# Performance work log

Measured on AMD Instinct MI355X. Metric: run time of the kernel, lower is better.

## Reference

```python
import jax, jax.numpy as jnp
import numpy as np

N, K, C, CL = 1024, 32, 64, 128
H = 2 * C  # MLP hidden = 2 * pair channels


def _ln(x, g, b, eps=1e-5):
    m = x.mean(-1, keepdims=True)
    v = jnp.mean(jnp.square(x - m), -1, keepdims=True)
    return (x - m) * jax.lax.rsqrt(v + eps) * g + b


def setup_inputs() -> dict:
    key = jax.random.key(0)
    ks = jax.random.split(key, 16)

    def w(k, shape):
        return jax.random.normal(k, shape, jnp.float32) / np.float32(np.sqrt(shape[0]))

    local = jax.random.normal(ks[0], (N, CL), jnp.float32)
    pair = jax.random.normal(ks[1], (N, N, C), jnp.float32)
    pair_update = jax.random.normal(ks[2], (N, K, C), jnp.float32)
    r = jax.random.randint(ks[3], (N, K), -(N // 4), N)
    neighbours = jnp.where(r < 0, -1, r)
    mask = jax.random.bernoulli(ks[4], 0.9, (N,))
    return dict(
        local=local, pair=pair, pair_update=pair_update,
        neighbours=neighbours, mask=mask,
        Wa=w(ks[5], (CL, C)), Wb=w(ks[6], (CL, C)),
        ln_g=jnp.ones((C,), jnp.float32), ln_b=jnp.zeros((C,), jnp.float32),
        W_aug=w(ks[7], (C, C)), W_lin=w(ks[8], (C, C)),
        W_left=w(ks[9], (C, 32)), b_left=jnp.zeros((32,), jnp.float32),
        W_right=w(ks[10], (C, 32)), b_right=jnp.zeros((32,), jnp.float32),
        W1=w(ks[11], (32, H)), W2=w(ks[12], (H, C)),
        W_int=w(ks[13], (CL, C)), b_int=jnp.zeros((C,), jnp.float32),
    )


def reference(local, pair, pair_update, neighbours, mask,
              Wa, Wb, ln_g, ln_b, W_aug, W_lin,
              W_left, b_left, W_right, b_right, W1, W2, W_int, b_int):
    idx = jnp.arange(pair.shape[0])
    # inject local info into the sparse pair update   [N,K,C]
    pu = pair_update + (local @ Wa)[:, None] + (local @ Wb)[neighbours]
    # gather neighbour pair features + layernorm      [N,K,C]
    lp = _ln(pair[idx[:, None], neighbours], ln_g, ln_b)
    lp = lp + pu @ W_aug
    linear = lp @ W_lin                               # [N,K,C]
    left = lp @ W_left + b_left                       # [N,K,32]
    right = lp @ W_right + b_right                    # [N,K,32]
    # neighbour-of-neighbour pair features            [N,K,K,32]
    npair = left[:, None] + right[neighbours]
    pn = neighbours[neighbours]                       # [N,K,K]
    pn = jnp.where((neighbours == -1)[:, :, None], pn, -1)
    pm = (pn != -1) & mask[pn] & (neighbours != -1)[:, None, :]
    # fused per-edge-pair MLP                          [N,K,K,C]
    upd = jax.nn.gelu(npair @ W1) @ W2
    # masked mean over the middle neighbour axis       [N,K,C]
    upd = jnp.where(pm[..., None], upd, 0.0).sum(axis=1)
    upd = upd / jnp.maximum(pm.sum(axis=1), 1).astype(upd.dtype)[..., None]
    inter = local @ W_int + b_int                     # [N,C]
    # scatter-add back into the dense pair tensor (collisions possible)
    return pair.at[idx[:, None], neighbours].add(upd + inter[:, None] + linear)
```

## Files before the change

### kernel.cpp

```cpp
#include <hip/hip_runtime.h>
#include <hip/hip_bf16.h>

constexpr int Nn  = 1024;
constexpr int Kk  = 32;
constexpr int Cc  = 64;
constexpr int CLl = 128;

typedef unsigned int   u32;
typedef unsigned short u16;
typedef float f4v __attribute__((ext_vector_type(4)));

__device__ __forceinline__ float gelu_tanh(float v){
  float c = 0.7978845608028654f*(v + 0.044715f*v*v*v);
  return 0.5f*v*(1.f + tanhf(c));
}
__device__ __forceinline__ float bflo(u32 u){ return __uint_as_float(u<<16); }
__device__ __forceinline__ float bfhi(u32 u){ return __uint_as_float(u & 0xffff0000u); }
__device__ __forceinline__ u32 pack_bf(float a, float b){
  u32 xa = __float_as_uint(a), xb = __float_as_uint(b);
  u32 ra = (xa + 0x7fffu + ((xa>>16)&1u)) >> 16;
  u32 rb = (xb + 0x7fffu + ((xb>>16)&1u)) >> 16;
  return ra | (rb<<16);
}

__global__ __launch_bounds__(64) void k0(
    const float* __restrict__ local, const float* __restrict__ Wa,
    const float* __restrict__ Wb, const float* __restrict__ Wint,
    const float* __restrict__ b_int,
    float* __restrict__ A, float* __restrict__ B, float* __restrict__ inter){
  int i = blockIdx.x;
  int c = threadIdx.x;
  __shared__ float l[CLl];
  l[c]      = local[i*CLl + c];
  l[c + 64] = local[i*CLl + 64 + c];
  __syncthreads();
  float a = 0.f, b = 0.f, t = 0.f;
  #pragma unroll 4
  for(int d = 0; d < CLl; ++d){
    float ld = l[d];
    a = fmaf(ld, Wa[d*Cc + c], a);
    b = fmaf(ld, Wb[d*Cc + c], b);
    t = fmaf(ld, Wint[d*Cc + c], t);
  }
  A[i*Cc + c] = a;
  B[i*Cc + c] = b;
  inter[i*Cc + c] = t + b_int[c];
}

__global__ __launch_bounds__(256) void k1(
    const float* __restrict__ pair, const float* __restrict__ pair_update,
    const int* __restrict__ neigh, const int* __restrict__ mask,
    const float* __restrict__ ln_g, const float* __restrict__ ln_b,
    const float* __restrict__ W_aug, const float* __restrict__ W_right,
    const float* __restrict__ b_right,
    const float* __restrict__ A, const float* __restrict__ B,
    float* __restrict__ r1023, int* __restrict__ qpart){
  const int i = Nn - 1;
  __shared__ float wA[4096];
  __shared__ float wR[2048];
  __shared__ float p [Kk][68];
  __shared__ float pu[Kk][68];
  __shared__ float lp[Kk][68];
  __shared__ int   nwS[Kk];
  __shared__ float ssum[Kk][9], ssq[Kk][9], stats[Kk][2];
  int tid = threadIdx.x;
  for(int idx = tid; idx < 4096; idx += 256) wA[idx] = W_aug[idx];
  for(int idx = tid; idx < 2048; idx += 256) wR[idx] = W_right[idx];
  if(tid < Kk){
    int n = neigh[i*Kk + tid];
    nwS[tid] = (n < 0) ? n + Nn : n;
    qpart[tid] = (n != -1 && mask[n] != 0) ? 1 : 0;
  }
  __syncthreads();
  int k = tid >> 3, s = tid & 7;
  {
    const float* prow = pair + ((size_t)i*Nn + nwS[k])*Cc + s*8;
    const float* pur  = pair_update + ((size_t)i*Kk + k)*Cc + s*8;
    const float* Ar = A + i*Cc + s*8;
    const float* Br = B + (size_t)nwS[k]*Cc + s*8;
    float ps = 0.f, ps2 = 0.f;
    for(int j = 0; j < 8; ++j){
      float v = prow[j];
      p[k][s*8 + j] = v; ps += v; ps2 += v*v;
      pu[k][s*8 + j] = pur[j] + Ar[j] + Br[j];
    }
    ssum[k][s] = ps; ssq[k][s] = ps2;
  }
  __syncthreads();
  if(s == 0){
    float m = 0.f, q = 0.f;
    for(int j = 0; j < 8; ++j){ m += ssum[k][j]; q += ssq[k][j]; }
    m *= (1.f/64.f); q *= (1.f/64.f);
    float var = fmaxf(q - m*m, 0.f);
    stats[k][0] = m; stats[k][1] = rsqrtf(var + 1e-5f);
  }
  __syncthreads();
  {
    float m = stats[k][0], r = stats[k][1];
    float acc[8];
    #pragma unroll
    for(int j = 0; j < 8; ++j){
      int c = s*8 + j;
      acc[j] = (p[k][c] - m)*r*ln_g[c] + ln_b[c];
    }
    for(int d = 0; d < 64; ++d){
      float pd = pu[k][d];
      #pragma unroll
      for(int j = 0; j < 8; ++j) acc[j] = fmaf(pd, wA[d*64 + s*8 + j], acc[j]);
    }
    #pragma unroll
    for(int j = 0; j < 8; ++j) lp[k][s*8 + j] = acc[j];
  }
  __syncthreads();
  {
    float acc[4] = {0.f,0.f,0.f,0.f};
    for(int d = 0; d < 64; ++d){
      float ld = lp[k][d];
      #pragma unroll
      for(int j = 0; j < 4; ++j) acc[j] = fmaf(ld, wR[d*32 + s*4 + j], acc[j]);
    }
    #pragma unroll
    for(int j = 0; j < 4; ++j)
      r1023[k*32 + s*4 + j] = acc[j] + b_right[s*4 + j];
  }
}

__global__ __launch_bounds__(256) void kbig(
    const float* __restrict__ pair, const float* __restrict__ pair_update,
    const int* __restrict__ neigh,
    const float* __restrict__ ln_g, const float* __restrict__ ln_b,
    const float* __restrict__ W_aug, const float* __restrict__ W_lin,
    const float* __restrict__ W_left, const float* __restrict__ b_left,
    const float* __restrict__ W1, const float* __restrict__ W2,
    const float* __restrict__ A, const float* __restrict__ B,
    const float* __restrict__ inter, const float* __restrict__ r1023,
    const int* __restrict__ qpart,
    float* __restrict__ out){

  __shared__ u32 wbA[2048];
  __shared__ u32 wbL[2048];
  __shared__ u32 wbF[1024];
  __shared__ u32 w1b[2048];
  __shared__ u32 w2b[4096];
  __shared__ float pbuf[Kk][68];
  __shared__ u32  puP [Kk][34];
  __shared__ float uA[1088];
  __shared__ float stats[Kk][2];
  __shared__ float AiS[64], InS[64], lgS[64], lbS[64];
  __shared__ int nbS[Kk], nwS[Kk], quS[Kk], leadS[Kk];
  __shared__ int cminus;

  float* ssum = uA;
  float* ssq  = uA + 288;
  float* hbuf = uA;

  const int i   = blockIdx.x;
  const int tid = threadIdx.x;

  const f4v* __restrict__ srcRow = (const f4v*)(pair + (size_t)i*Nn*Cc);
  f4v* __restrict__       dstRow = (f4v*)(out + (size_t)i*Nn*Cc);

  #pragma unroll 4
  for(int it = 0; it < 32; ++it){
    int idx = it*256 + tid;
    dstRow[idx] = srcRow[idx];
  }

  for(int idx = tid; idx < 2048; idx += 256){
    const float2 wa = *(const float2*)(W_aug + idx*2);
    wbA[idx] = pack_bf(wa.x, wa.y);
    const float2 wl = *(const float2*)(W_lin + idx*2);
    wbL[idx] = pack_bf(wl.x, wl.y);
    const float2 w1 = *(const float2*)(W1 + idx*2);
    w1b[idx] = pack_bf(w1.x, w1.y);
    const float2 w2a = *(const float2*)(W2 + idx*2);
    w2b[idx] = pack_bf(w2a.x, w2a.y);
    const float2 w2c = *(const float2*)(W2 + 4096 + idx*2);
    w2b[2048 + idx] = pack_bf(w2c.x, w2c.y);
  }
  for(int idx = tid; idx < 1024; idx += 256){
    const float2 wf = *(const float2*)(W_left + idx*2);
    wbF[idx] = pack_bf(wf.x, wf.y);
  }
  if(tid < Kk){
    int n = neigh[i*Kk + tid];
    nbS[tid] = n;
    nwS[tid] = (n < 0) ? n + Nn : n;
    quS[tid] = qpart[tid];
  }
  if(tid < 64){
    AiS[tid] = A[i*Cc + tid];
    InS[tid] = inter[i*Cc + tid];
    lgS[tid] = ln_g[tid];
    lbS[tid] = ln_b[tid];
  }
  __syncthreads();

  if(tid == 0){
    int c = 0;
    for(int kk = 0; kk < Kk; ++kk) c |= (nbS[kk] == -1);
    cminus = c;
  }
  if(tid < Kk){
    int lead = 1;
    for(int kk = 0; kk < tid; ++kk) if(nwS[kk] == nwS[tid]) lead = 0;
    leadS[tid] = lead;
  }

  {
    int k8 = tid >> 3, s8 = tid & 7;
    const float4* p4 = (const float4*)(pair + ((size_t)i*Nn + nwS[k8])*Cc) + s8*2;
    float4 p0 = p4[0], p1 = p4[1];
    const float4* u4 = (const float4*)(pair_update + ((size_t)i*Kk + k8)*Cc) + s8*2;
    float4 u0 = u4[0], u1 = u4[1];
    const float4* Br = (const float4*)(B + (size_t)nwS[k8]*Cc) + s8*2;
    float4 b0 = Br[0], b1 = Br[1];
    float pf[8] = {p0.x,p0.y,p0.z,p0.w,p1.x,p1.y,p1.z,p1.w};
    float uf[8] = {u0.x,u0.y,u0.z,u0.w,u1.x,u1.y,u1.z,u1.w};
    float bv[8] = {b0.x,b0.y,b0.z,b0.w,b1.x,b1.y,b1.z,b1.w};
    float ps = 0.f, ps2 = 0.f;
    #pragma unroll
    for(int j = 0; j < 8; ++j){
      float v = pf[j];
      pbuf[k8][s8*8 + j] = v; ps += v; ps2 += v*v;
    }
    #pragma unroll
    for(int j = 0; j < 4; ++j){
      float e0 = uf[2*j]   + AiS[s8*8 + 2*j]   + bv[2*j];
      float e1 = uf[2*j+1] + AiS[s8*8 + 2*j+1] + bv[2*j+1];
      puP[k8][s8*4 + j] = pack_bf(e0, e1);
    }
    ssum[k8*9 + s8] = ps; ssq[k8*9 + s8] = ps2;
  }
  __syncthreads();

  if((tid & 7) == 0){
    int k8 = tid >> 3;
    float m = 0.f, q = 0.f;
    for(int j = 0; j < 8; ++j){ m += ssum[k8*9 + j]; q += ssq[k8*9 + j]; }
    m *= (1.f/64.f); q *= (1.f/64.f);
    float var = fmaxf(q - m*m, 0.f);
    stats[k8][0] = m; stats[k8][1] = rsqrtf(var + 1e-5f);
  }
  __syncthreads();

  const int kq  = tid >> 4;
  const int s   = tid & 15;
  const int k0i = kq, k1i = kq + 16;
  const int c0  = s*4;

  float a0[4], a1[4];
  {
    float m0 = stats[k0i][0], r0 = stats[k0i][1];
    float m1 = stats[k1i][0], r1 = stats[k1i][1];
    #pragma unroll
    for(int j = 0; j < 4; ++j){
      int c = c0 + j;
      a0[j] = (pbuf[k0i][c] - m0)*r0*lgS[c] + lbS[c];
      a1[j] = (pbuf[k1i][c] - m1)*r1*lgS[c] + lbS[c];
    }
    #pragma unroll 2
    for(int dp = 0; dp < 32; ++dp){
      u32 q0 = puP[k0i][dp], q1 = puP[k1i][dp];
      float pe0 = bflo(q0), po0 = bfhi(q0);
      float pe1 = bflo(q1), po1 = bfhi(q1);
      uint2 we = *(const uint2*)&wbA[(2*dp)*32 + s*2];
      uint2 wo = *(const uint2*)&wbA[(2*dp+1)*32 + s*2];
      float w0 = bflo(we.x), w1 = bfhi(we.x), w2 = bflo(we.y), w3 = bfhi(we.y);
      a0[0] = fmaf(pe0, w0, a0[0]); a0[1] = fmaf(pe0, w1, a0[1]);
      a0[2] = fmaf(pe0, w2, a0[2]); a0[3] = fmaf(pe0, w3, a0[3]);
      a1[0] = fmaf(pe1, w0, a1[0]); a1[1] = fmaf(pe1, w1, a1[1]);
      a1[2] = fmaf(pe1, w2, a1[2]); a1[3] = fmaf(pe1, w3, a1[3]);
      float x0w = bflo(wo.x), x1w = bfhi(wo.x), x2w = bflo(wo.y), x3w = bfhi(wo.y);
      a0[0] = fmaf(po0, x0w, a0[0]); a0[1] = fmaf(po0, x1w, a0[1]);
      a0[2] = fmaf(po0, x2w, a0[2]); a0[3] = fmaf(po0, x3w, a0[3]);
      a1[0] = fmaf(po1, x0w, a1[0]); a1[1] = fmaf(po1, x1w, a1[1]);
      a1[2] = fmaf(po1, x2w, a1[2]); a1[3] = fmaf(po1, x3w, a1[3]);
    }
  }
  __syncthreads();
  #pragma unroll
  for(int j = 0; j < 4; ++j){ pbuf[k0i][c0 + j] = a0[j]; pbuf[k1i][c0 + j] = a1[j]; }

  #pragma unroll 4
  for(int it = 32; it < 48; ++it){
    int idx = it*256 + tid;
    dstRow[idx] = srcRow[idx];
  }
  __syncthreads();

  float L0[4], L1[4];
  {
    float Lx0[4] = {0,0,0,0}, Lx1[4] = {0,0,0,0};
    float X0[2] = {0,0}, X1[2] = {0,0};
    #pragma unroll 4
    for(int d = 0; d < 64; ++d){
      float p0 = pbuf[k0i][d], p1 = pbuf[k1i][d];
      uint2 wv = *(const uint2*)&wbL[d*32 + s*2];
      float w0 = bflo(wv.x), w1 = bfhi(wv.x), w2 = bflo(wv.y), w3 = bfhi(wv.y);
      Lx0[0] = fmaf(p0, w0, Lx0[0]); Lx0[1] = fmaf(p0, w1, Lx0[1]);
      Lx0[2] = fmaf(p0, w2, Lx0[2]); Lx0[3] = fmaf(p0, w3, Lx0[3]);
      Lx1[0] = fmaf(p1, w0, Lx1[0]); Lx1[1] = fmaf(p1, w1, Lx1[1]);
      Lx1[2] = fmaf(p1, w2, Lx1[2]); Lx1[3] = fmaf(p1, w3, Lx1[3]);
      u32 wf = wbF[d*16 + s];
      float f0 = bflo(wf), f1 = bfhi(wf);
      X0[0] = fmaf(p0, f0, X0[0]); X0[1] = fmaf(p0, f1, X0[1]);
      X1[0] = fmaf(p1, f0, X1[0]); X1[1] = fmaf(p1, f1, X1[1]);
    }
    #pragma unroll
    for(int j = 0; j < 4; ++j){
      L0[j] = Lx0[j] + InS[c0 + j];
      L1[j] = Lx1[j] + InS[c0 + j];
    }
    int x0 = s*2;
    float2 bl = *(const float2*)(b_left + x0);
    float2 rA = *(const float2*)(r1023 + k0i*32 + x0);
    float2 rB = *(const float2*)(r1023 + k1i*32 + x0);
    hbuf[k0i*34 + x0]     = X0[0] + bl.x + rA.x;
    hbuf[k0i*34 + x0 + 1] = X0[1] + bl.y + rA.y;
    hbuf[k1i*34 + x0]     = X1[0] + bl.x + rB.x;
    hbuf[k1i*34 + x0 + 1] = X1[1] + bl.y + rB.y;
  }
  #pragma unroll 4
  for(int it = 48; it < 64; ++it){
    int idx = it*256 + tid;
    dstRow[idx] = srcRow[idx];
  }
  __syncthreads();

  float g0[8], g1v[8];
  {
    float A0[8] = {0,0,0,0,0,0,0,0}, A1[8] = {0,0,0,0,0,0,0,0};
    #pragma unroll 2
    for(int x = 0; x < 32; ++x){
      float h0 = hbuf[k0i*34 + x], h1 = hbuf[k1i*34 + x];
      uint4 wv = *(const uint4*)&w1b[x*64 + s*4];
      float w[8] = {bflo(wv.x),bfhi(wv.x),bflo(wv.y),bfhi(wv.y),
                    bflo(wv.z),bfhi(wv.z),bflo(wv.w),bfhi(wv.w)};
      #pragma unroll
      for(int j = 0; j < 8; ++j){
        A0[j] = fmaf(h0, w[j], A0[j]);
        A1[j] = fmaf(h1, w[j], A1[j]);
      }
    }
    #pragma unroll
    for(int j = 0; j < 8; ++j){ g0[j] = gelu_tanh(A0[j]); g1v[j] = gelu_tanh(A1[j]); }
  }
  {
    float V0[4] = {0,0,0,0}, V1[4] = {0,0,0,0};
    int lbase = (kq & 3) << 4;
    for(int hb = 0; hb < 16; ++hb){
      int srcl = lbase | hb;
      #pragma unroll
      for(int hj = 0; hj < 8; ++hj){
        float gA = __shfl(g0[hj],  srcl, 64);
        float gB = __shfl(g1v[hj], srcl, 64);
        int h = hb*8 + hj;
        uint2 wv = *(const uint2*)&w2b[h*32 + s*2];
        float w0 = bflo(wv.x), w1 = bfhi(wv.x), w2 = bflo(wv.y), w3 = bfhi(wv.y);
        V0[0] = fmaf(gA, w0, V0[0]); V0[1] = fmaf(gA, w1, V0[1]);
        V0[2] = fmaf(gA, w2, V0[2]); V0[3] = fmaf(gA, w3, V0[3]);
        V1[0] = fmaf(gB, w0, V1[0]); V1[1] = fmaf(gB, w1, V1[1]);
        V1[2] = fmaf(gB, w2, V1[2]); V1[3] = fmaf(gB, w3, V1[3]);
      }
    }
    float mul0 = (cminus && quS[k0i] && nbS[k0i] != -1) ? 1.f : 0.f;
    float mul1 = (cminus && quS[k1i] && nbS[k1i] != -1) ? 1.f : 0.f;
    #pragma unroll
    for(int j = 0; j < 4; ++j){
      pbuf[k0i][c0 + j] = fmaf(mul0, V0[j], L0[j]);
      pbuf[k1i][c0 + j] = fmaf(mul1, V1[j], L1[j]);
    }
  }
  __syncthreads();

  {
    int k8 = tid >> 3, s8 = tid & 7;
    if(leadS[k8]){
      int col = nwS[k8];
      float tot[8] = {0,0,0,0,0,0,0,0};
      for(int kk = 0; kk < Kk; ++kk){
        if(nwS[kk] == col){
          #pragma unroll
          for(int j = 0; j < 8; ++j) tot[j] += pbuf[kk][s8*8 + j];
        }
      }
      size_t base = ((size_t)i*Nn + col)*Cc + s8*8;
      const float4* pv = (const float4*)(pair + base);
      float4 p0 = pv[0], p1 = pv[1];
      float4 o0 = make_float4(p0.x+tot[0], p0.y+tot[1], p0.z+tot[2], p0.w+tot[3]);
      float4 o1 = make_float4(p1.x+tot[4], p1.y+tot[5], p1.z+tot[6], p1.w+tot[7]);
      float4* ov = (float4*)(out + base);
      ov[0] = o0; ov[1] = o1;
    }
  }
}

extern "C" void kernel_launch(void* const* d_in, const int* in_sizes, int n_in,
                              void* d_out, int out_size, void* d_ws, size_t ws_size,
                              hipStream_t stream){
  (void)in_sizes; (void)n_in; (void)out_size; (void)ws_size;
  const float* local       = (const float*)d_in[0];
  const float* pair        = (const float*)d_in[1];
  const float* pair_update = (const float*)d_in[2];
  const int*   neighbours  = (const int*)d_in[3];
  const int*   mask        = (const int*)d_in[4];
  const float* Wa          = (const float*)d_in[5];
  const float* Wb          = (const float*)d_in[6];
  const float* ln_g        = (const float*)d_in[7];
  const float* ln_b        = (const float*)d_in[8];
  const float* W_aug       = (const float*)d_in[9];
  const float* W_lin       = (const float*)d_in[10];
  const float* W_left      = (const float*)d_in[11];
  const float* b_left      = (const float*)d_in[12];
  const float* W_right     = (const float*)d_in[13];
  const float* b_right     = (const float*)d_in[14];
  const float* W1          = (const float*)d_in[15];
  const float* W2          = (const float*)d_in[16];
  const float* W_int       = (const float*)d_in[17];
  const float* b_int       = (const float*)d_in[18];

  float* ws    = (float*)d_ws;
  float* A     = ws;
  float* B     = ws + 65536;
  float* inter = ws + 131072;
  float* r1023 = ws + 196608;
  int*   qpart = (int*)(ws + 197632);

  k0<<<dim3(Nn), dim3(64), 0, stream>>>(local, Wa, Wb, W_int, b_int, A, B, inter);
  k1<<<dim3(1), dim3(256), 0, stream>>>(pair, pair_update, neighbours, mask,
                                        ln_g, ln_b, W_aug, W_right, b_right,
                                        A, B, r1023, qpart);
  kbig<<<dim3(Nn), dim3(256), 0, stream>>>(pair, pair_update, neighbours,
                                           ln_g, ln_b, W_aug, W_lin,
                                           W_left, b_left, W1, W2,
                                           A, B, inter, r1023, qpart,
                                           (float*)d_out);
}
```

Measured before the change: 526.5 us.

## Split dense pair copy into standalone nontemporal copy kernel fused with projections

The bulk copy of `pair` into the output moves out of the main per-row compute kernel into a new grid-wide kernel. That kernel uses nontemporal vector loads and stores and also computes the local projections (A, B, inter) that k0 used to do. The compute kernel now only writes the scattered rows, and it reuses the gathered pair values already held in registers instead of reloading them from global memory. The aim is to let the copy stream at full bandwidth without competing with compute for LDS and registers. The cost is that the copy no longer overlaps with compute inside one kernel, so the two phases now run one after the other.

```diff
diff --git a/kernel.cpp b/kernel.cpp
--- a/kernel.cpp
+++ b/kernel.cpp
@@ -23,28 +23,43 @@
   return ra | (rb<<16);
 }
 
-__global__ __launch_bounds__(64) void k0(
+__global__ __launch_bounds__(256) void kcopy(
+    const f4v* __restrict__ src, f4v* __restrict__ dst,
     const float* __restrict__ local, const float* __restrict__ Wa,
     const float* __restrict__ Wb, const float* __restrict__ Wint,
     const float* __restrict__ b_int,
     float* __restrict__ A, float* __restrict__ B, float* __restrict__ inter){
-  int i = blockIdx.x;
-  int c = threadIdx.x;
-  __shared__ float l[CLl];
-  l[c]      = local[i*CLl + c];
-  l[c + 64] = local[i*CLl + 64 + c];
-  __syncthreads();
-  float a = 0.f, b = 0.f, t = 0.f;
-  #pragma unroll 4
-  for(int d = 0; d < CLl; ++d){
-    float ld = l[d];
-    a = fmaf(ld, Wa[d*Cc + c], a);
-    b = fmaf(ld, Wb[d*Cc + c], b);
-    t = fmaf(ld, Wint[d*Cc + c], t);
-  }
-  A[i*Cc + c] = a;
-  B[i*Cc + c] = b;
-  inter[i*Cc + c] = t + b_int[c];
+  const int tid = threadIdx.x;
+  size_t base = (size_t)blockIdx.x * (256*32) + tid;
+  #pragma unroll
+  for(int g = 0; g < 4; ++g){
+    f4v v[8];
+    #pragma unroll
+    for(int j = 0; j < 8; ++j)
+      v[j] = __builtin_nontemporal_load(&src[base + (size_t)(g*8 + j)*256]);
+    #pragma unroll
+    for(int j = 0; j < 8; ++j)
+      __builtin_nontemporal_store(v[j], &dst[base + (size_t)(g*8 + j)*256]);
+  }
+  if(blockIdx.x < (unsigned)Nn){
+    __shared__ float l[CLl];
+    if(tid < CLl) l[tid] = local[blockIdx.x*CLl + tid];
+    __syncthreads();
+    if(tid < 64){
+      const int c = tid, i = blockIdx.x;
+      float a = 0.f, b = 0.f, t = 0.f;
+      #pragma unroll 4
+      for(int d = 0; d < CLl; ++d){
+        float ld = l[d];
+        a = fmaf(ld, Wa[d*Cc + c], a);
+        b = fmaf(ld, Wb[d*Cc + c], b);
+        t = fmaf(ld, Wint[d*Cc + c], t);
+      }
+      A[i*Cc + c] = a;
+      B[i*Cc + c] = b;
+      inter[i*Cc + c] = t + b_int[c];
+    }
+  }
 }
 
 __global__ __launch_bounds__(256) void k1(
@@ -125,7 +140,7 @@
   }
 }
 
-__global__ __launch_bounds__(256) void kbig(
+__global__ __launch_bounds__(256) void kcomp(
     const float* __restrict__ pair, const float* __restrict__ pair_update,
     const int* __restrict__ neigh,
     const float* __restrict__ ln_g, const float* __restrict__ ln_b,
@@ -157,15 +172,6 @@
   const int i   = blockIdx.x;
   const int tid = threadIdx.x;
 
-  const f4v* __restrict__ srcRow = (const f4v*)(pair + (size_t)i*Nn*Cc);
-  f4v* __restrict__       dstRow = (f4v*)(out + (size_t)i*Nn*Cc);
-
-  #pragma unroll 4
-  for(int it = 0; it < 32; ++it){
-    int idx = it*256 + tid;
-    dstRow[idx] = srcRow[idx];
-  }
-
   for(int idx = tid; idx < 2048; idx += 256){
     const float2 wa = *(const float2*)(W_aug + idx*2);
     wbA[idx] = pack_bf(wa.x, wa.y);
@@ -207,6 +213,7 @@
     leadS[tid] = lead;
   }
 
+  float pf[8];
   {
     int k8 = tid >> 3, s8 = tid & 7;
     const float4* p4 = (const float4*)(pair + ((size_t)i*Nn + nwS[k8])*Cc) + s8*2;
@@ -215,7 +222,8 @@
     float4 u0 = u4[0], u1 = u4[1];
     const float4* Br = (const float4*)(B + (size_t)nwS[k8]*Cc) + s8*2;
     float4 b0 = Br[0], b1 = Br[1];
-    float pf[8] = {p0.x,p0.y,p0.z,p0.w,p1.x,p1.y,p1.z,p1.w};
+    pf[0]=p0.x; pf[1]=p0.y; pf[2]=p0.z; pf[3]=p0.w;
+    pf[4]=p1.x; pf[5]=p1.y; pf[6]=p1.z; pf[7]=p1.w;
     float uf[8] = {u0.x,u0.y,u0.z,u0.w,u1.x,u1.y,u1.z,u1.w};
     float bv[8] = {b0.x,b0.y,b0.z,b0.w,b1.x,b1.y,b1.z,b1.w};
     float ps = 0.f, ps2 = 0.f;
@@ -281,12 +289,6 @@
   __syncthreads();
   #pragma unroll
   for(int j = 0; j < 4; ++j){ pbuf[k0i][c0 + j] = a0[j]; pbuf[k1i][c0 + j] = a1[j]; }
-
-  #pragma unroll 4
-  for(int it = 32; it < 48; ++it){
-    int idx = it*256 + tid;
-    dstRow[idx] = srcRow[idx];
-  }
   __syncthreads();
 
   float L0[4], L1[4];
@@ -320,11 +322,6 @@
     hbuf[k0i*34 + x0 + 1] = X0[1] + bl.y + rA.y;
     hbuf[k1i*34 + x0]     = X1[0] + bl.x + rB.x;
     hbuf[k1i*34 + x0 + 1] = X1[1] + bl.y + rB.y;
-  }
-  #pragma unroll 4
-  for(int it = 48; it < 64; ++it){
-    int idx = it*256 + tid;
-    dstRow[idx] = srcRow[idx];
   }
   __syncthreads();
 
@@ -386,10 +383,8 @@
         }
       }
       size_t base = ((size_t)i*Nn + col)*Cc + s8*8;
-      const float4* pv = (const float4*)(pair + base);
-      float4 p0 = pv[0], p1 = pv[1];
-      float4 o0 = make_float4(p0.x+tot[0], p0.y+tot[1], p0.z+tot[2], p0.w+tot[3]);
-      float4 o1 = make_float4(p1.x+tot[4], p1.y+tot[5], p1.z+tot[6], p1.w+tot[7]);
+      float4 o0 = make_float4(pf[0]+tot[0], pf[1]+tot[1], pf[2]+tot[2], pf[3]+tot[3]);
+      float4 o1 = make_float4(pf[4]+tot[4], pf[5]+tot[5], pf[6]+tot[6], pf[7]+tot[7]);
       float4* ov = (float4*)(out + base);
       ov[0] = o0; ov[1] = o1;
     }
@@ -427,13 +422,15 @@
   float* r1023 = ws + 196608;
   int*   qpart = (int*)(ws + 197632);
 
-  k0<<<dim3(Nn), dim3(64), 0, stream>>>(local, Wa, Wb, W_int, b_int, A, B, inter);
+  kcopy<<<dim3(2048), dim3(256), 0, stream>>>(
+      (const f4v*)pair, (f4v*)d_out,
+      local, Wa, Wb, W_int, b_int, A, B, inter);
   k1<<<dim3(1), dim3(256), 0, stream>>>(pair, pair_update, neighbours, mask,
                                         ln_g, ln_b, W_aug, W_right, b_right,
                                         A, B, r1023, qpart);
-  kbig<<<dim3(Nn), dim3(256), 0, stream>>>(pair, pair_update, neighbours,
-                                           ln_g, ln_b, W_aug, W_lin,
-                                           W_left, b_left, W1, W2,
-                                           A, B, inter, r1023, qpart,
-                                           (float*)d_out);
-}
+  kcomp<<<dim3(Nn), dim3(256), 0, stream>>>(pair, pair_update, neighbours,
+                                            ln_g, ln_b, W_aug, W_lin,
+                                            W_left, b_left, W1, W2,
+                                            A, B, inter, r1023, qpart,
+                                            (float*)d_out);
+}
```

Result: slower. 540.5 us (+2.6%).
